# Performance work log

Measured on AMD Instinct MI355X. Metric: run time of the kernel, lower is better.

The kernel has to match this reference:

```python
import jax, jax.numpy as jnp
import numpy as np

NHEAD = 16
EPS_ATTN = 1e-6
EPS_LN = 1e-5


def _layer_norm(x, g, b):
    mu = jnp.mean(x, -1, keepdims=True)
    var = jnp.mean((x - mu) ** 2, -1, keepdims=True)
    return (x - mu) * jax.lax.rsqrt(var + EPS_LN) * g + b


def _run_layer(x, S_prev, z_prev, lp, m):
    # x: (B,E); S_prev: (B,H,D,D); z_prev: (B,H,D,1); m: (B,1,1) or None
    qkv_w, qkv_b, out_w, out_b, n1g, n1b, n2g, n2b, f1w, f1b, f2w, f2b = lp
    B, E = x.shape
    H = NHEAD
    D = E // H
    qkv = x @ qkv_w.T + qkv_b
    q, k, v = [t.reshape(B, H, D) for t in jnp.split(qkv, 3, -1)]
    q = jax.nn.elu(q) + 1.0
    k = jax.nn.elu(k) + 1.0
    if m is not None:
        k = k * m
        v = v * m
    S_new = S_prev + jnp.einsum('bhd,bhm->bhdm', k, v)
    z_new = z_prev + k[..., None]
    num = jnp.einsum('bhd,bhdm->bhm', q, S_new)
    den = jnp.einsum('bhd,bhd->bh', q, z_new[..., 0])[..., None]
    attn = (num / (den + EPS_ATTN)).reshape(B, E)
    x = _layer_norm(x + attn @ out_w.T + out_b, n1g, n1b)
    h = jax.nn.relu(x @ f1w.T + f1b) @ f2w.T + f2b
    x = _layer_norm(x + h, n2g, n2b)
    return x, S_new, z_new


def _scan_layers(x_t, Ss, zs, params, m):
    # params: tuple of arrays each with leading layer dim L
    def body(x, xs):
        lp, S, z = xs
        x, S, z = _run_layer(x, S, z, lp, m)
        return x, (S, z)
    x_out, (Ss_new, zs_new) = jax.lax.scan(body, x_t, (params, Ss, zs))
    return x_out, Ss_new, zs_new


def _forward(x, lengths, out_lengths, emb_w, emb_b, enc_p, dec_p, fc_p):
    B, Slen, _ = x.shape
    E = emb_w.shape[0]
    H = NHEAD
    D = E // H
    L = enc_p[0].shape[0]
    h = x @ emb_w.T + emb_b
    # sinusoidal positional encoding
    pos = jnp.arange(Slen, dtype=h.dtype)[:, None]
    div = jnp.exp(jnp.arange(0, E, 2, dtype=h.dtype) * (-np.log(10000.0) / E))
    pe = jnp.zeros((Slen, E), h.dtype)
    pe = pe.at[:, 0::2].set(jnp.sin(pos * div)).at[:, 1::2].set(jnp.cos(pos * div))
    h = h + pe[None]
    mask = (jnp.arange(Slen)[None, :] < lengths[:, None]).astype(h.dtype)  # (B,S)
    Ss0 = jnp.zeros((L, B, H, D, D), h.dtype)
    zs0 = jnp.zeros((L, B, H, D, 1), h.dtype)

    def enc_step(carry, inp):
        Ss, zs, _ = carry
        x_t, m_t = inp
        x_out, Ss, zs = _scan_layers(x_t, Ss, zs, enc_p, m_t[:, None, None])
        return (Ss, zs, x_out), None

    (Ss, zs, x_last), _ = jax.lax.scan(
        enc_step, (Ss0, zs0, jnp.zeros((B, E), h.dtype)),
        (h.transpose(1, 0, 2), mask.T))

    fc1_w, fc1_b, fc2_w, fc2_b = fc_p

    def dec_step(carry, _):
        xd, Ss, zs = carry
        xd, Ss, zs = _scan_layers(xd, Ss, zs, dec_p, None)
        out = jax.nn.relu(xd @ fc1_w.T + fc1_b) @ fc2_w.T + fc2_b
        return (xd, Ss, zs), out

    _, outs = jax.lax.scan(dec_step, (x_last, Ss, zs), None, length=out_lengths)
    return outs.transpose(1, 0, 2)  # (B, out_lengths, num_classes)


def setup_inputs() -> dict:
    key = jax.random.key(0)
    B, S, IN, E, L, C, TOUT = 4, 256, 256, 1024, 4, 1000, 32
    ks = iter(jax.random.split(key, 64))

    def w(shape, s=0.02):
        return jax.random.normal(next(ks), shape, jnp.float32) * s

    d = {}
    d['x'] = jax.random.normal(next(ks), (B, S, IN), jnp.float32)
    d['lengths'] = jax.random.randint(next(ks), (B,), 1, S + 1)
    d['out_lengths'] = TOUT
    d['emb_w'] = w((E, IN))
    d['emb_b'] = jnp.zeros((E,), jnp.float32)
    for pre in ('enc', 'dec'):
        d[f'{pre}_qkv_w'] = w((L, 3 * E, E))
        d[f'{pre}_qkv_b'] = jnp.zeros((L, 3 * E), jnp.float32)
        d[f'{pre}_out_w'] = w((L, E, E))
        d[f'{pre}_out_b'] = jnp.zeros((L, E), jnp.float32)
        d[f'{pre}_n1g'] = jnp.ones((L, E), jnp.float32)
        d[f'{pre}_n1b'] = jnp.zeros((L, E), jnp.float32)
        d[f'{pre}_n2g'] = jnp.ones((L, E), jnp.float32)
        d[f'{pre}_n2b'] = jnp.zeros((L, E), jnp.float32)
        d[f'{pre}_f1w'] = w((L, E, E))  # dim_feedforward == hidden_size
        d[f'{pre}_f1b'] = jnp.zeros((L, E), jnp.float32)
        d[f'{pre}_f2w'] = w((L, E, E))
        d[f'{pre}_f2b'] = jnp.zeros((L, E), jnp.float32)
    d['fc1_w'] = w((E, E))
    d['fc1_b'] = jnp.zeros((E,), jnp.float32)
    d['fc2_w'] = w((C, E))
    d['fc2_b'] = jnp.zeros((C,), jnp.float32)
    return d


def reference(x, lengths, out_lengths, emb_w, emb_b,
              enc_qkv_w, enc_qkv_b, enc_out_w, enc_out_b, enc_n1g, enc_n1b,
              enc_n2g, enc_n2b, enc_f1w, enc_f1b, enc_f2w, enc_f2b,
              dec_qkv_w, dec_qkv_b, dec_out_w, dec_out_b, dec_n1g, dec_n1b,
              dec_n2g, dec_n2b, dec_f1w, dec_f1b, dec_f2w, dec_f2b,
              fc1_w, fc1_b, fc2_w, fc2_b):
    enc_p = (enc_qkv_w, enc_qkv_b, enc_out_w, enc_out_b, enc_n1g, enc_n1b,
             enc_n2g, enc_n2b, enc_f1w, enc_f1b, enc_f2w, enc_f2b)
    dec_p = (dec_qkv_w, dec_qkv_b, dec_out_w, dec_out_b, dec_n1g, dec_n1b,
             dec_n2g, dec_n2b, dec_f1w, dec_f1b, dec_f2w, dec_f2b)
    fc_p = (fc1_w, fc1_b, fc2_w, fc2_b)
    return _forward(x, lengths, out_lengths, emb_w, emb_b, enc_p, dec_p, fc_p)
```

## Files before the change

kernel.cpp:

```cpp
#include <hip/hip_runtime.h>
#include <hip/hip_bf16.h>
#include <cstdint>


#define EP_NONE     0
#define EP_PE       1
#define EP_QKV      2
#define EP_RELU     3
#define EP_RES      4

__device__ __forceinline__ float bf2f(unsigned short s) {
    union { unsigned u; float f; } t; t.u = ((unsigned)s) << 16; return t.f;
}
__device__ __forceinline__ unsigned short f2bf(float f) {
    union { float f; unsigned u; } t; t.f = f;
    unsigned u = t.u;
    unsigned r = u + 0x7FFFu + ((u >> 16) & 1u);
    return (unsigned short)(r >> 16);
}
__device__ __forceinline__ float ldS(const void* p, size_t i, bool b) {
    return b ? bf2f(((const unsigned short*)p)[i]) : ((const float*)p)[i];
}
__device__ __forceinline__ void ld4d(const void* p, size_t i, bool b, float o[4]) {
    if (b) {
        ushort4 v = *(const ushort4*)((const unsigned short*)p + i);
        o[0] = bf2f(v.x); o[1] = bf2f(v.y); o[2] = bf2f(v.z); o[3] = bf2f(v.w);
    } else {
        float4 v = *(const float4*)((const float*)p + i);
        o[0] = v.x; o[1] = v.y; o[2] = v.z; o[3] = v.w;
    }
}
__device__ __forceinline__ void stS(void* p, size_t i, bool b, float v) {
    if (b) ((unsigned short*)p)[i] = f2bf(v);
    else   ((float*)p)[i] = v;
}

__global__ void detect_k(const unsigned* __restrict__ ones,
                         const int* __restrict__ lens, int* __restrict__ flag)
{
    if (threadIdx.x == 0 && blockIdx.x == 0) {
        flag[0] = (ones[0] == 0x3F803F80u) ? 1 : 0;
        flag[1] = (lens[1] == 0 && lens[3] == 0) ? 1 : 0;
    }
}

template <int EPI>
__global__ __launch_bounds__(256) void gemm_k(
    const void* __restrict__ A, int a_ext, int t0, int chb,
    const void* __restrict__ W, size_t woff,
    const void* __restrict__ bias, size_t boff,
    const float* __restrict__ res, float* __restrict__ C,
    int M, int N, int K,
    const int* __restrict__ lengths, const int* __restrict__ flag)
{
    const bool ebf = flag[0] != 0;
    const bool abf = ebf && (a_ext != 0);
    __shared__ float Asm[16][64];
    __shared__ float Wsm[16][64];
    const int tid = threadIdx.x;
    const int tn = tid & 15, tm = tid >> 4;
    const int n0 = blockIdx.x * 64, m0 = blockIdx.y * 64;
    const int chm = (1 << chb) - 1;
    float acc[4][4] = {};

    const int lr = tid >> 2;
    const int lc = (tid & 3) << 2;
    const int lrow = m0 + lr;
    const size_t arow = a_ext ? ((size_t)(lrow >> chb) * 256 + t0 + (lrow & chm))
                              : (size_t)lrow;
    const size_t abase = arow * K + lc;
    const size_t wbase = woff + (size_t)(n0 + lr) * K + lc;

    for (int k0 = 0; k0 < K; k0 += 16) {
        float av[4], wv[4];
        ld4d(A, abase + k0, abf, av);
        ld4d(W, wbase + k0, ebf, wv);
        Asm[lc + 0][lr] = av[0]; Asm[lc + 1][lr] = av[1];
        Asm[lc + 2][lr] = av[2]; Asm[lc + 3][lr] = av[3];
        Wsm[lc + 0][lr] = wv[0]; Wsm[lc + 1][lr] = wv[1];
        Wsm[lc + 2][lr] = wv[2]; Wsm[lc + 3][lr] = wv[3];
        __syncthreads();
#pragma unroll
        for (int kk = 0; kk < 16; ++kk) {
            float4 a4 = *(const float4*)&Asm[kk][tm << 2];
            float4 w4 = *(const float4*)&Wsm[kk][tn << 2];
            float ar[4] = {a4.x, a4.y, a4.z, a4.w};
            float wr[4] = {w4.x, w4.y, w4.z, w4.w};
#pragma unroll
            for (int i = 0; i < 4; ++i)
#pragma unroll
                for (int j = 0; j < 4; ++j)
                    acc[i][j] += ar[i] * wr[j];
        }
        __syncthreads();
    }

    const int row = m0 + (tm << 2);
    const int col = n0 + (tn << 2);
#pragma unroll
    for (int i = 0; i < 4; ++i) {
        int r = row + i;
        float vr[4];
#pragma unroll
        for (int j = 0; j < 4; ++j) {
            int c = col + j;
            float v = acc[i][j] + ldS(bias, boff + c, ebf);
            if constexpr (EPI == EP_PE) {
                int t = t0 + (r & chm);
                float freq = expf((float)(c & ~1) * (-9.210340371976184f / 1024.0f));
                float ang = (float)t * freq;
                v += (c & 1) ? cosf(ang) : sinf(ang);
            } else if constexpr (EPI == EP_QKV) {
                if (c < 2048)
                    v = v > 0.f ? v + 1.f : expf(v);
                if (c >= 1024) {
                    int bb = r >> chb, t = t0 + (r & chm);
                    int len = lengths[flag[1] ? (bb << 1) : bb];
                    if (t >= len) v = 0.f;
                }
            } else if constexpr (EPI == EP_RELU) {
                v = fmaxf(v, 0.f);
            } else if constexpr (EPI == EP_RES) {
                v += res[(size_t)r * N + c];
            }
            vr[j] = v;
        }
        *(float4*)&C[(size_t)r * N + col] = *(float4*)vr;
    }
}

__global__ __launch_bounds__(64) void enc_attn_k(
    const float* __restrict__ qkvc, float* __restrict__ attnc,
    float* __restrict__ Sst, float* __restrict__ zst, int first, int CH)
{
    const int bid = blockIdx.x;
    const int mg = bid & 3, h = (bid >> 2) & 15, b = bid >> 6;
    const int bh = b * 16 + h;
    const int tid = threadIdx.x;
    const int ml = tid & 15, d4 = tid >> 4, db = d4 << 4;
    const int m = (mg << 4) + ml;

    float Sa[16], za[16];
    if (first) {
#pragma unroll
        for (int j = 0; j < 16; ++j) { Sa[j] = 0.f; za[j] = 0.f; }
    } else {
#pragma unroll
        for (int j = 0; j < 16; ++j) {
            Sa[j] = Sst[(size_t)bh * 4096 + (size_t)(db + j) * 64 + m];
            za[j] = zst[(size_t)bh * 64 + db + j];
        }
    }

    __shared__ float ks[32][64];
    __shared__ float qs[32][64];
    __shared__ float vs[32][16];

    for (int s = 0; s < CH; s += 32) {
        __syncthreads();
        for (int r = 0; r < 32; ++r) {
            const float* p = qkvc + (size_t)(b * CH + s + r) * 3072 + (h << 6);
            qs[r][tid] = p[tid];
            ks[r][tid] = p[1024 + tid];
        }
        for (int i = tid; i < 512; i += 64) {
            int r = i >> 4, c = i & 15;
            vs[r][c] = qkvc[(size_t)(b * CH + s + r) * 3072 + 2048 + (h << 6) + (mg << 4) + c];
        }
        __syncthreads();

        for (int tt = 0; tt < 32; ++tt) {
            float v = vs[tt][ml];
            const float4* k4 = (const float4*)&ks[tt][db];
            const float4* q4 = (const float4*)&qs[tt][db];
            float pn = 0.f, pd = 0.f;
#pragma unroll
            for (int j = 0; j < 4; ++j) {
                float4 kk = k4[j], qq = q4[j];
                Sa[4*j+0] += kk.x * v; za[4*j+0] += kk.x;
                Sa[4*j+1] += kk.y * v; za[4*j+1] += kk.y;
                Sa[4*j+2] += kk.z * v; za[4*j+2] += kk.z;
                Sa[4*j+3] += kk.w * v; za[4*j+3] += kk.w;
                pn += qq.x*Sa[4*j+0] + qq.y*Sa[4*j+1] + qq.z*Sa[4*j+2] + qq.w*Sa[4*j+3];
                pd += qq.x*za[4*j+0] + qq.y*za[4*j+1] + qq.z*za[4*j+2] + qq.w*za[4*j+3];
            }
            pn += __shfl_xor(pn, 16); pd += __shfl_xor(pd, 16);
            pn += __shfl_xor(pn, 32); pd += __shfl_xor(pd, 32);
            if (d4 == 0)
                attnc[(size_t)(b * CH + s + tt) * 1024 + (h << 6) + m] = pn / (pd + 1e-6f);
        }
    }

#pragma unroll
    for (int j = 0; j < 16; ++j)
        Sst[(size_t)bh * 4096 + (size_t)(db + j) * 64 + m] = Sa[j];
    if (ml == 0) {
#pragma unroll
        for (int j = 0; j < 16; ++j)
            zst[(size_t)bh * 64 + db + j] = za[j];
    }
}

__global__ __launch_bounds__(256) void ln_k(
    float* __restrict__ Y, const void* __restrict__ g, size_t goff,
    const void* __restrict__ b, size_t boff, const int* __restrict__ flag)
{
    const bool ebf = flag[0] != 0;
    __shared__ float red[256];
    const int row = blockIdx.x, tid = threadIdx.x;
    float4* y4 = (float4*)(Y + (size_t)row * 1024);
    float4 x = y4[tid];
    red[tid] = x.x + x.y + x.z + x.w;
    __syncthreads();
    for (int o = 128; o > 0; o >>= 1) {
        if (tid < o) red[tid] += red[tid + o];
        __syncthreads();
    }
    float mu = red[0] * (1.0f / 1024.0f);
    __syncthreads();
    float dx = x.x - mu, dy = x.y - mu, dz = x.z - mu, dw = x.w - mu;
    red[tid] = dx * dx + dy * dy + dz * dz + dw * dw;
    __syncthreads();
    for (int o = 128; o > 0; o >>= 1) {
        if (tid < o) red[tid] += red[tid + o];
        __syncthreads();
    }
    float rs = rsqrtf(red[0] * (1.0f / 1024.0f) + 1e-5f);
    float gv[4], bv[4];
    ld4d(g, goff + (size_t)tid * 4, ebf, gv);
    ld4d(b, boff + (size_t)tid * 4, ebf, bv);
    float4 o;
    o.x = dx * rs * gv[0] + bv[0];
    o.y = dy * rs * gv[1] + bv[1];
    o.z = dz * rs * gv[2] + bv[2];
    o.w = dw * rs * gv[3] + bv[3];
    y4[tid] = o;
}

template <int EPI, bool XN, int RES, bool ODYN>
__global__ __launch_bounds__(256) void sgemm2_k(
    const float* __restrict__ x,
    const void* __restrict__ lxg, size_t lxgo,
    const void* __restrict__ lxb, size_t lxbo,
    const float* __restrict__ res,
    const void* __restrict__ lrg, size_t lrgo,
    const void* __restrict__ lrb, size_t lrbo,
    const void* __restrict__ W, size_t woff,
    const void* __restrict__ bias, size_t boff,
    void* __restrict__ C, int N, int K, int ldc, int coff,
    const int* __restrict__ flag)
{
    const bool ebf = flag[0] != 0;
    const int wv = threadIdx.x >> 6, lane = threadIdx.x & 63;
    __shared__ float sxm[4], sxr[4], srm[4], srr[4];

    if (XN) {
        const float4* xr = (const float4*)(x + (size_t)wv * K);
        float s = 0.f, q = 0.f;
        for (int i = lane; i < (K >> 2); i += 64) {
            float4 v = xr[i];
            s += v.x + v.y + v.z + v.w;
            q += v.x*v.x + v.y*v.y + v.z*v.z + v.w*v.w;
        }
        for (int o2 = 32; o2; o2 >>= 1) { s += __shfl_xor(s, o2); q += __shfl_xor(q, o2); }
        if (lane == 0) {
            float mu = s / (float)K;
            sxm[wv] = mu;
            sxr[wv] = rsqrtf(q / (float)K - mu * mu + 1e-5f);
        }
    }
    if (RES == 2) {
        const float4* rr = (const float4*)(res + (size_t)wv * N);
        float s = 0.f, q = 0.f;
        for (int i = lane; i < (N >> 2); i += 64) {
            float4 v = rr[i];
            s += v.x + v.y + v.z + v.w;
            q += v.x*v.x + v.y*v.y + v.z*v.z + v.w*v.w;
        }
        for (int o2 = 32; o2; o2 >>= 1) { s += __shfl_xor(s, o2); q += __shfl_xor(q, o2); }
        if (lane == 0) {
            float mu = s / (float)N;
            srm[wv] = mu;
            srr[wv] = rsqrtf(q / (float)N - mu * mu + 1e-5f);
        }
    }
    if (XN || RES == 2) __syncthreads();

    const int n = blockIdx.x * 4 + wv;
    const size_t wbase = woff + (size_t)n * K;
    const float4* x0 = (const float4*)(x);
    const float4* x1 = (const float4*)(x + K);
    const float4* x2 = (const float4*)(x + 2 * K);
    const float4* x3 = (const float4*)(x + 3 * K);
    float m0=0,r0=1,m1=0,r1=1,m2=0,r2=1,m3=0,r3=1;
    if (XN) {
        m0 = sxm[0]; r0 = sxr[0]; m1 = sxm[1]; r1 = sxr[1];
        m2 = sxm[2]; r2 = sxr[2]; m3 = sxm[3]; r3 = sxr[3];
    }
    float a0 = 0.f, a1 = 0.f, a2 = 0.f, a3 = 0.f;
    for (int i = lane; i < (K >> 2); i += 64) {
        float w[4];
        ld4d(W, wbase + (size_t)i * 4, ebf, w);
        float g[4], be[4];
        if (XN) {
            ld4d(lxg, lxgo + (size_t)i * 4, ebf, g);
            ld4d(lxb, lxbo + (size_t)i * 4, ebf, be);
        }
        float4 v;
#define ROWACC(XP, ACC, MU, RS)                                               \
        v = XP[i];                                                            \
        if (XN) {                                                             \
            ACC += ((v.x - MU) * RS * g[0] + be[0]) * w[0]                    \
                 + ((v.y - MU) * RS * g[1] + be[1]) * w[1]                    \
                 + ((v.z - MU) * RS * g[2] + be[2]) * w[2]                    \
                 + ((v.w - MU) * RS * g[3] + be[3]) * w[3];                   \
        } else {                                                              \
            ACC += v.x * w[0] + v.y * w[1] + v.z * w[2] + v.w * w[3];         \
        }
        ROWACC(x0, a0, m0, r0)
        ROWACC(x1, a1, m1, r1)
        ROWACC(x2, a2, m2, r2)
        ROWACC(x3, a3, m3, r3)
#undef ROWACC
    }
    for (int o2 = 32; o2; o2 >>= 1) {
        a0 += __shfl_down(a0, o2);
        a1 += __shfl_down(a1, o2);
        a2 += __shfl_down(a2, o2);
        a3 += __shfl_down(a3, o2);
    }
    if (lane == 0) {
        float bn = ldS(bias, boff + n, ebf);
        float v[4] = {a0 + bn, a1 + bn, a2 + bn, a3 + bn};
        float rg = 0.f, rb = 0.f;
        if (RES == 2) { rg = ldS(lrg, lrgo + n, ebf); rb = ldS(lrb, lrbo + n, ebf); }
#pragma unroll
        for (int b2 = 0; b2 < 4; ++b2) {
            if constexpr (RES == 1) {
                v[b2] += res[(size_t)b2 * N + n];
            } else if constexpr (RES == 2) {
                v[b2] += (res[(size_t)b2 * N + n] - srm[b2]) * srr[b2] * rg + rb;
            }
            if constexpr (EPI == EP_QKV) {
                if (n < 2048) v[b2] = v[b2] > 0.f ? v[b2] + 1.f : expf(v[b2]);
            } else if constexpr (EPI == EP_RELU) {
                v[b2] = fmaxf(v[b2], 0.f);
            }
            size_t idx = (size_t)coff + (size_t)b2 * ldc + n;
            if constexpr (ODYN) stS(C, idx, ebf, v[b2]);
            else                ((float*)C)[idx] = v[b2];
        }
    }
}

__global__ __launch_bounds__(64) void dec_attn_k(
    const float* __restrict__ qkv, float* __restrict__ Sst,
    float* __restrict__ zst, float* __restrict__ attn)
{
    const int bh = blockIdx.x;
    const int b = bh >> 4, h = bh & 15;
    const int lane = threadIdx.x;
    const float* base = qkv + (size_t)b * 3072 + (h << 6);
    float q = base[lane];
    float k = base[1024 + lane];
    float v = base[2048 + lane];
    __shared__ float kq[128];
    kq[lane] = k;
    kq[64 + lane] = q;
    float* zp = zst + (size_t)bh * 64;
    float zn = zp[lane] + k;
    zp[lane] = zn;
    float p = q * zn;
    for (int off = 32; off; off >>= 1) p += __shfl_xor(p, off);
    float den = p + 1e-6f;
    __syncthreads();
    float* Sp = Sst + (size_t)bh * 4096;
    float num = 0.f;
#pragma unroll 8
    for (int d = 0; d < 64; ++d) {
        float s = Sp[d * 64 + lane] + kq[d] * v;
        Sp[d * 64 + lane] = s;
        num += kq[64 + d] * s;
    }
    attn[(size_t)b * 1024 + (h << 6) + lane] = num / den;
}

__global__ __launch_bounds__(256) void copy_last_k(
    const float* __restrict__ Xc, float* __restrict__ xd, int CH)
{
    int i = blockIdx.x * 256 + threadIdx.x;
    int b = i >> 10, e = i & 1023;
    xd[i] = Xc[(size_t)(b * CH + CH - 1) * 1024 + e];
}

extern "C" void kernel_launch(void* const* d_in, const int* in_sizes, int n_in,
                              void* d_out, int out_size, void* d_ws, size_t ws_size,
                              hipStream_t stream)
{
    (void)n_in; (void)out_size;
    constexpr int E = 1024, B = 4, L = 4, TOUT = 32, NC = 1000;

    const int CH  = (ws_size >= (size_t)30 * 1024 * 1024) ? 256 : 32;
    const int chb = (CH == 256) ? 8 : 5;
    const int NCH = 256 / CH;
    const int MC  = B * CH;

    const int o = (in_sizes[2] == 1) ? 0 : -1;

    const void* x_in = d_in[0];
    const int*  lens = (const int*)d_in[1];
    const void* emb_w = d_in[3 + o];
    const void* emb_b = d_in[4 + o];
    const void* e_qkv_w = d_in[5 + o];  const void* e_qkv_b = d_in[6 + o];
    const void* e_out_w = d_in[7 + o];  const void* e_out_b = d_in[8 + o];
    const void* e_n1g = d_in[9 + o];    const void* e_n1b = d_in[10 + o];
    const void* e_n2g = d_in[11 + o];   const void* e_n2b = d_in[12 + o];
    const void* e_f1w = d_in[13 + o];   const void* e_f1b = d_in[14 + o];
    const void* e_f2w = d_in[15 + o];   const void* e_f2b = d_in[16 + o];
    const void* d_qkv_w = d_in[17 + o]; const void* d_qkv_b = d_in[18 + o];
    const void* d_out_w = d_in[19 + o]; const void* d_out_b = d_in[20 + o];
    const void* d_n1g = d_in[21 + o];   const void* d_n1b = d_in[22 + o];
    const void* d_n2g = d_in[23 + o];   const void* d_n2b = d_in[24 + o];
    const void* d_f1w = d_in[25 + o];   const void* d_f1b = d_in[26 + o];
    const void* d_f2w = d_in[27 + o];   const void* d_f2b = d_in[28 + o];
    const void* fc1_w = d_in[29 + o];   const void* fc1_b = d_in[30 + o];
    const void* fc2_w = d_in[31 + o];   const void* fc2_b = d_in[32 + o];

    float* wsf   = (float*)d_ws;
    int*   flag  = (int*)d_ws;
    float* u     = wsf + 64;
    float* t1    = u + B * E;
    float* qkvd  = t1 + B * E;
    float* attnd = qkvd + B * 3 * E;
    float* hfd   = attnd + B * E;
    float* Xc    = hfd + B * E;
    float* Yc    = Xc + (size_t)MC * E;
    float* attnc = Yc + (size_t)MC * E;
    float* qkvc  = attnc + (size_t)MC * E;
    float* zs    = qkvc + (size_t)MC * 3 * E;
    float* Ss    = zs + (size_t)L * B * 16 * 64;
    float* Hc    = qkvc;

    const size_t SstL = (size_t)B * 16 * 64 * 64;
    const size_t zstL = (size_t)B * 16 * 64;

    detect_k<<<1, 64, 0, stream>>>((const unsigned*)e_n1g, lens, flag);

    for (int c = 0; c < NCH; ++c) {
        const int t0 = c * CH;
        gemm_k<EP_PE><<<dim3(E / 64, MC / 64), 256, 0, stream>>>(
            x_in, 1, t0, chb, emb_w, 0, emb_b, 0, nullptr, Xc,
            MC, E, 256, lens, flag);

        for (int l = 0; l < L; ++l) {
            const size_t qw_o = (size_t)l * 3 * E * E, qb_o = (size_t)l * 3 * E;
            const size_t ow_o = (size_t)l * E * E,     ob_o = (size_t)l * E;
            const size_t fw_o = (size_t)l * E * E,     fb_o = (size_t)l * E;
            const size_t g_o  = (size_t)l * E;

            gemm_k<EP_QKV><<<dim3(3 * E / 64, MC / 64), 256, 0, stream>>>(
                Xc, 0, t0, chb, e_qkv_w, qw_o, e_qkv_b, qb_o, nullptr, qkvc,
                MC, 3 * E, E, lens, flag);
            enc_attn_k<<<B * 16 * 4, 64, 0, stream>>>(
                qkvc, attnc, Ss + l * SstL, zs + l * zstL, c == 0 ? 1 : 0, CH);
            gemm_k<EP_RES><<<dim3(E / 64, MC / 64), 256, 0, stream>>>(
                attnc, 0, t0, chb, e_out_w, ow_o, e_out_b, ob_o, Xc, Yc,
                MC, E, E, lens, flag);
            ln_k<<<MC, 256, 0, stream>>>(Yc, e_n1g, g_o, e_n1b, g_o, flag);
            gemm_k<EP_RELU><<<dim3(E / 64, MC / 64), 256, 0, stream>>>(
                Yc, 0, t0, chb, e_f1w, fw_o, e_f1b, fb_o, nullptr, Hc,
                MC, E, E, lens, flag);
            gemm_k<EP_RES><<<dim3(E / 64, MC / 64), 256, 0, stream>>>(
                Hc, 0, t0, chb, e_f2w, fw_o, e_f2b, fb_o, Yc, Xc,
                MC, E, E, lens, flag);
            ln_k<<<MC, 256, 0, stream>>>(Xc, e_n2g, g_o, e_n2b, g_o, flag);
        }
    }

    copy_last_k<<<16, 256, 0, stream>>>(Xc, u, CH);

    for (int t = 0; t < TOUT; ++t) {
        for (int l = 0; l < L; ++l) {
            const size_t qw_o = (size_t)l * 3 * E * E, qb_o = (size_t)l * 3 * E;
            const size_t ow_o = (size_t)l * E * E,     ob_o = (size_t)l * E;
            const size_t fw_o = (size_t)l * E * E,     fb_o = (size_t)l * E;
            const size_t g_o  = (size_t)l * E;
            const size_t pg_o = (size_t)((l == 0) ? 3 : (l - 1)) * E;

            if (t == 0 && l == 0)
                sgemm2_k<EP_QKV, false, 0, false><<<3 * E / 4, 256, 0, stream>>>(
                    u, nullptr, 0, nullptr, 0, nullptr, nullptr, 0, nullptr, 0,
                    d_qkv_w, qw_o, d_qkv_b, qb_o, qkvd, 3 * E, E, 3 * E, 0, flag);
            else
                sgemm2_k<EP_QKV, true, 0, false><<<3 * E / 4, 256, 0, stream>>>(
                    u, d_n2g, pg_o, d_n2b, pg_o, nullptr, nullptr, 0, nullptr, 0,
                    d_qkv_w, qw_o, d_qkv_b, qb_o, qkvd, 3 * E, E, 3 * E, 0, flag);

            dec_attn_k<<<B * 16, 64, 0, stream>>>(
                qkvd, Ss + l * SstL, zs + l * zstL, attnd);

            if (t == 0 && l == 0)
                sgemm2_k<EP_NONE, false, 1, false><<<E / 4, 256, 0, stream>>>(
                    attnd, nullptr, 0, nullptr, 0, u, nullptr, 0, nullptr, 0,
                    d_out_w, ow_o, d_out_b, ob_o, t1, E, E, E, 0, flag);
            else
                sgemm2_k<EP_NONE, false, 2, false><<<E / 4, 256, 0, stream>>>(
                    attnd, nullptr, 0, nullptr, 0, u, d_n2g, pg_o, d_n2b, pg_o,
                    d_out_w, ow_o, d_out_b, ob_o, t1, E, E, E, 0, flag);

            sgemm2_k<EP_RELU, true, 0, false><<<E / 4, 256, 0, stream>>>(
                t1, d_n1g, g_o, d_n1b, g_o, nullptr, nullptr, 0, nullptr, 0,
                d_f1w, fw_o, d_f1b, fb_o, hfd, E, E, E, 0, flag);

            sgemm2_k<EP_NONE, false, 2, false><<<E / 4, 256, 0, stream>>>(
                hfd, nullptr, 0, nullptr, 0, t1, d_n1g, g_o, d_n1b, g_o,
                d_f2w, fw_o, d_f2b, fb_o, u, E, E, E, 0, flag);
        }
        sgemm2_k<EP_RELU, true, 0, false><<<E / 4, 256, 0, stream>>>(
            u, d_n2g, (size_t)3 * E, d_n2b, (size_t)3 * E,
            nullptr, nullptr, 0, nullptr, 0,
            fc1_w, 0, fc1_b, 0, hfd, E, E, E, 0, flag);
        sgemm2_k<EP_NONE, false, 0, true><<<NC / 4, 256, 0, stream>>>(
            hfd, nullptr, 0, nullptr, 0, nullptr, nullptr, 0, nullptr, 0,
            fc2_w, 0, fc2_b, 0, d_out, NC, E, TOUT * NC, t * NC, flag);
    }
}
```

Measured before the change: 6.153 ms.

## Use bf16 MFMA with hi/lo split for encoder chunk GEMMs

Replaces the scalar FP32 shared-memory tiled GEMM in the encoder with an MFMA 16x16x32 bf16 kernel. FP32 operands are split into high and low bf16 parts and combined over three MFMA passes to keep near-FP32 accuracy. When weights are already bf16, the extra low-part passes are skipped. This trades extra conversion work and scalar, uncoalesced epilogue stores for matrix-core throughput.

New measurement: 5.739 ms. 6.7% less time.

```diff
diff --git a/kernel.cpp b/kernel.cpp
--- a/kernel.cpp
+++ b/kernel.cpp
@@ -8,6 +8,10 @@
 #define EP_QKV      2
 #define EP_RELU     3
 #define EP_RES      4
+
+typedef __attribute__((ext_vector_type(8))) short bf8v;
+typedef __attribute__((ext_vector_type(8))) unsigned short us8;
+typedef __attribute__((ext_vector_type(4))) float f4_t;
 
 __device__ __forceinline__ float bf2f(unsigned short s) {
     union { unsigned u; float f; } t; t.u = ((unsigned)s) << 16; return t.f;
@@ -35,6 +39,19 @@
     else   ((float*)p)[i] = v;
 }
 
+__device__ __forceinline__ void split_store(unsigned short* hp, unsigned short* lp,
+                                            const float fv[8]) {
+    us8 h, l;
+#pragma unroll
+    for (int i = 0; i < 8; ++i) {
+        unsigned short hh = f2bf(fv[i]);
+        h[i] = (short)hh;
+        l[i] = f2bf(fv[i] - bf2f(hh));
+    }
+    *(us8*)hp = h;
+    *(us8*)lp = l;
+}
+
 __global__ void detect_k(const unsigned* __restrict__ ones,
                          const int* __restrict__ lens, int* __restrict__ flag)
 {
@@ -45,7 +62,7 @@
 }
 
 template <int EPI>
-__global__ __launch_bounds__(256) void gemm_k(
+__global__ __launch_bounds__(256) void mgemm_k(
     const void* __restrict__ A, int a_ext, int t0, int chb,
     const void* __restrict__ W, size_t woff,
     const void* __restrict__ bias, size_t boff,
@@ -53,79 +70,120 @@
     int M, int N, int K,
     const int* __restrict__ lengths, const int* __restrict__ flag)
 {
+    (void)M;
     const bool ebf = flag[0] != 0;
     const bool abf = ebf && (a_ext != 0);
-    __shared__ float Asm[16][64];
-    __shared__ float Wsm[16][64];
+    __shared__ __align__(16) unsigned short Ah[64][40];
+    __shared__ __align__(16) unsigned short Al[64][40];
+    __shared__ __align__(16) unsigned short Bh[64][40];
+    __shared__ __align__(16) unsigned short Bl[64][40];
+
     const int tid = threadIdx.x;
-    const int tn = tid & 15, tm = tid >> 4;
-    const int n0 = blockIdx.x * 64, m0 = blockIdx.y * 64;
+    const int n0 = blockIdx.x << 6, m0 = blockIdx.y << 6;
     const int chm = (1 << chb) - 1;
-    float acc[4][4] = {};
-
-    const int lr = tid >> 2;
-    const int lc = (tid & 3) << 2;
-    const int lrow = m0 + lr;
-    const size_t arow = a_ext ? ((size_t)(lrow >> chb) * 256 + t0 + (lrow & chm))
-                              : (size_t)lrow;
-    const size_t abase = arow * K + lc;
-    const size_t wbase = woff + (size_t)(n0 + lr) * K + lc;
-
-    for (int k0 = 0; k0 < K; k0 += 16) {
-        float av[4], wv[4];
-        ld4d(A, abase + k0, abf, av);
-        ld4d(W, wbase + k0, ebf, wv);
-        Asm[lc + 0][lr] = av[0]; Asm[lc + 1][lr] = av[1];
-        Asm[lc + 2][lr] = av[2]; Asm[lc + 3][lr] = av[3];
-        Wsm[lc + 0][lr] = wv[0]; Wsm[lc + 1][lr] = wv[1];
-        Wsm[lc + 2][lr] = wv[2]; Wsm[lc + 3][lr] = wv[3];
+
+    const int srow = tid >> 2;
+    const int sc0 = (tid & 3) << 3;
+    const int lrowA = m0 + srow;
+    const size_t arow = a_ext ? ((size_t)(lrowA >> chb) * 256 + t0 + (lrowA & chm))
+                              : (size_t)lrowA;
+    const size_t abase = arow * (size_t)K + sc0;
+    const size_t wbase = woff + (size_t)(n0 + srow) * K + sc0;
+
+    const int lane = tid & 63;
+    const int wv4 = tid >> 6;
+    const int wm = (wv4 >> 1) << 5;
+    const int wn = (wv4 & 1) << 5;
+    const int fr = lane & 15;
+    const int fk = (lane >> 4) << 3;
+
+    f4_t a00 = {}, a01 = {}, a10 = {}, a11 = {};
+
+    for (int k0 = 0; k0 < K; k0 += 32) {
+        if (abf) {
+            const unsigned short* ap = (const unsigned short*)A + abase + k0;
+            *(us8*)&Ah[srow][sc0] = *(const us8*)ap;
+            us8 z = {};
+            *(us8*)&Al[srow][sc0] = z;
+        } else {
+            const float* ap = (const float*)A + abase + k0;
+            float4 f0 = *(const float4*)ap;
+            float4 f1 = *(const float4*)(ap + 4);
+            float fv[8] = {f0.x, f0.y, f0.z, f0.w, f1.x, f1.y, f1.z, f1.w};
+            split_store(&Ah[srow][sc0], &Al[srow][sc0], fv);
+        }
+        if (ebf) {
+            const unsigned short* wp = (const unsigned short*)W + wbase + k0;
+            *(us8*)&Bh[srow][sc0] = *(const us8*)wp;
+        } else {
+            const float* wp = (const float*)W + wbase + k0;
+            float4 f0 = *(const float4*)wp;
+            float4 f1 = *(const float4*)(wp + 4);
+            float fv[8] = {f0.x, f0.y, f0.z, f0.w, f1.x, f1.y, f1.z, f1.w};
+            split_store(&Bh[srow][sc0], &Bl[srow][sc0], fv);
+        }
         __syncthreads();
-#pragma unroll
-        for (int kk = 0; kk < 16; ++kk) {
-            float4 a4 = *(const float4*)&Asm[kk][tm << 2];
-            float4 w4 = *(const float4*)&Wsm[kk][tn << 2];
-            float ar[4] = {a4.x, a4.y, a4.z, a4.w};
-            float wr[4] = {w4.x, w4.y, w4.z, w4.w};
-#pragma unroll
-            for (int i = 0; i < 4; ++i)
-#pragma unroll
-                for (int j = 0; j < 4; ++j)
-                    acc[i][j] += ar[i] * wr[j];
+
+        bf8v ah0 = *(const bf8v*)&Ah[wm + fr][fk];
+        bf8v ah1 = *(const bf8v*)&Ah[wm + 16 + fr][fk];
+        bf8v bh0 = *(const bf8v*)&Bh[wn + fr][fk];
+        bf8v bh1 = *(const bf8v*)&Bh[wn + 16 + fr][fk];
+        a00 = __builtin_amdgcn_mfma_f32_16x16x32_bf16(ah0, bh0, a00, 0, 0, 0);
+        a01 = __builtin_amdgcn_mfma_f32_16x16x32_bf16(ah0, bh1, a01, 0, 0, 0);
+        a10 = __builtin_amdgcn_mfma_f32_16x16x32_bf16(ah1, bh0, a10, 0, 0, 0);
+        a11 = __builtin_amdgcn_mfma_f32_16x16x32_bf16(ah1, bh1, a11, 0, 0, 0);
+        if (!abf) {
+            bf8v al0 = *(const bf8v*)&Al[wm + fr][fk];
+            bf8v al1 = *(const bf8v*)&Al[wm + 16 + fr][fk];
+            a00 = __builtin_amdgcn_mfma_f32_16x16x32_bf16(al0, bh0, a00, 0, 0, 0);
+            a01 = __builtin_amdgcn_mfma_f32_16x16x32_bf16(al0, bh1, a01, 0, 0, 0);
+            a10 = __builtin_amdgcn_mfma_f32_16x16x32_bf16(al1, bh0, a10, 0, 0, 0);
+            a11 = __builtin_amdgcn_mfma_f32_16x16x32_bf16(al1, bh1, a11, 0, 0, 0);
+        }
+        if (!ebf) {
+            bf8v bl0 = *(const bf8v*)&Bl[wn + fr][fk];
+            bf8v bl1 = *(const bf8v*)&Bl[wn + 16 + fr][fk];
+            a00 = __builtin_amdgcn_mfma_f32_16x16x32_bf16(ah0, bl0, a00, 0, 0, 0);
+            a01 = __builtin_amdgcn_mfma_f32_16x16x32_bf16(ah0, bl1, a01, 0, 0, 0);
+            a10 = __builtin_amdgcn_mfma_f32_16x16x32_bf16(ah1, bl0, a10, 0, 0, 0);
+            a11 = __builtin_amdgcn_mfma_f32_16x16x32_bf16(ah1, bl1, a11, 0, 0, 0);
         }
         __syncthreads();
     }
 
-    const int row = m0 + (tm << 2);
-    const int col = n0 + (tn << 2);
-#pragma unroll
-    for (int i = 0; i < 4; ++i) {
-        int r = row + i;
-        float vr[4];
-#pragma unroll
-        for (int j = 0; j < 4; ++j) {
-            int c = col + j;
-            float v = acc[i][j] + ldS(bias, boff + c, ebf);
-            if constexpr (EPI == EP_PE) {
-                int t = t0 + (r & chm);
-                float freq = expf((float)(c & ~1) * (-9.210340371976184f / 1024.0f));
-                float ang = (float)t * freq;
-                v += (c & 1) ? cosf(ang) : sinf(ang);
-            } else if constexpr (EPI == EP_QKV) {
-                if (c < 2048)
-                    v = v > 0.f ? v + 1.f : expf(v);
-                if (c >= 1024) {
-                    int bb = r >> chb, t = t0 + (r & chm);
-                    int len = lengths[flag[1] ? (bb << 1) : bb];
-                    if (t >= len) v = 0.f;
+    f4_t accs[2][2] = {{a00, a01}, {a10, a11}};
+    const int rb = m0 + wm + ((lane >> 4) << 2);
+    const int cb = n0 + wn + fr;
+#pragma unroll
+    for (int i = 0; i < 2; ++i) {
+#pragma unroll
+        for (int e = 0; e < 4; ++e) {
+            const int r = rb + i * 16 + e;
+#pragma unroll
+            for (int j = 0; j < 2; ++j) {
+                const int c = cb + j * 16;
+                float v = accs[i][j][e] + ldS(bias, boff + c, ebf);
+                if constexpr (EPI == EP_PE) {
+                    int t = t0 + (r & chm);
+                    float freq = expf((float)(c & ~1) * (-9.210340371976184f / 1024.0f));
+                    float ang = (float)t * freq;
+                    v += (c & 1) ? cosf(ang) : sinf(ang);
+                } else if constexpr (EPI == EP_QKV) {
+                    if (c < 2048)
+                        v = v > 0.f ? v + 1.f : expf(v);
+                    if (c >= 1024) {
+                        int bb = r >> chb, t = t0 + (r & chm);
+                        int len = lengths[flag[1] ? (bb << 1) : bb];
+                        if (t >= len) v = 0.f;
+                    }
+                } else if constexpr (EPI == EP_RELU) {
+                    v = fmaxf(v, 0.f);
+                } else if constexpr (EPI == EP_RES) {
+                    v += res[(size_t)r * N + c];
                 }
-            } else if constexpr (EPI == EP_RELU) {
-                v = fmaxf(v, 0.f);
-            } else if constexpr (EPI == EP_RES) {
-                v += res[(size_t)r * N + c];
+                C[(size_t)r * N + c] = v;
             }
-            vr[j] = v;
-        }
-        *(float4*)&C[(size_t)r * N + col] = *(float4*)vr;
+        }
     }
 }
 
@@ -448,7 +506,7 @@
 
     for (int c = 0; c < NCH; ++c) {
         const int t0 = c * CH;
-        gemm_k<EP_PE><<<dim3(E / 64, MC / 64), 256, 0, stream>>>(
+        mgemm_k<EP_PE><<<dim3(E / 64, MC / 64), 256, 0, stream>>>(
             x_in, 1, t0, chb, emb_w, 0, emb_b, 0, nullptr, Xc,
             MC, E, 256, lens, flag);
 
@@ -458,19 +516,19 @@
             const size_t fw_o = (size_t)l * E * E,     fb_o = (size_t)l * E;
             const size_t g_o  = (size_t)l * E;
 
-            gemm_k<EP_QKV><<<dim3(3 * E / 64, MC / 64), 256, 0, stream>>>(
+            mgemm_k<EP_QKV><<<dim3(3 * E / 64, MC / 64), 256, 0, stream>>>(
                 Xc, 0, t0, chb, e_qkv_w, qw_o, e_qkv_b, qb_o, nullptr, qkvc,
                 MC, 3 * E, E, lens, flag);
             enc_attn_k<<<B * 16 * 4, 64, 0, stream>>>(
                 qkvc, attnc, Ss + l * SstL, zs + l * zstL, c == 0 ? 1 : 0, CH);
-            gemm_k<EP_RES><<<dim3(E / 64, MC / 64), 256, 0, stream>>>(
+            mgemm_k<EP_RES><<<dim3(E / 64, MC / 64), 256, 0, stream>>>(
                 attnc, 0, t0, chb, e_out_w, ow_o, e_out_b, ob_o, Xc, Yc,
                 MC, E, E, lens, flag);
             ln_k<<<MC, 256, 0, stream>>>(Yc, e_n1g, g_o, e_n1b, g_o, flag);
-            gemm_k<EP_RELU><<<dim3(E / 64, MC / 64), 256, 0, stream>>>(
+            mgemm_k<EP_RELU><<<dim3(E / 64, MC / 64), 256, 0, stream>>>(
                 Yc, 0, t0, chb, e_f1w, fw_o, e_f1b, fb_o, nullptr, Hc,
                 MC, E, E, lens, flag);
-            gemm_k<EP_RES><<<dim3(E / 64, MC / 64), 256, 0, stream>>>(
+            mgemm_k<EP_RES><<<dim3(E / 64, MC / 64), 256, 0, stream>>>(
                 Hc, 0, t0, chb, e_f2w, fw_o, e_f2b, fb_o, Yc, Xc,
                 MC, E, E, lens, flag);
             ln_k<<<MC, 256, 0, stream>>>(Xc, e_n2g, g_o, e_n2b, g_o, flag);
```
